# Optimization experiments

Hardware: AMD Instinct MI355X
Metric: run time of the kernel (lower is better)

The kernel has to match this reference:

```python
import jax, jax.numpy as jnp
import numpy as np

B, H, W, DIM, HEADS, WS, SHIFT, MLP_RATIO = 32, 56, 56, 256, 8, 7, 3, 4
N = WS * WS                      # tokens per window = 49
NW = (H // WS) * (W // WS)       # windows per image = 64
HEAD_DIM = DIM // HEADS
HIDDEN = DIM * MLP_RATIO


def _rel_index():
    # standard Swin relative position index, shape (N, N), values in [0, (2*WS-1)^2)
    coords = np.stack(np.meshgrid(np.arange(WS), np.arange(WS), indexing='ij')).reshape(2, -1)
    rel = (coords[:, :, None] - coords[:, None, :]).transpose(1, 2, 0)
    rel[:, :, 0] += WS - 1
    rel[:, :, 1] += WS - 1
    rel[:, :, 0] *= 2 * WS - 1
    return rel.sum(-1).astype(np.int32)


def _attn_mask():
    # shifted-window attention mask, shape (NW, N, N), values in {0, -100}
    img = np.zeros((H, W))
    slices = (slice(0, -WS), slice(-WS, -SHIFT), slice(-SHIFT, None))
    cnt = 0
    for hs in slices:
        for ws_ in slices:
            img[hs, ws_] = cnt
            cnt += 1
    mw = img.reshape(H // WS, WS, W // WS, WS).transpose(0, 2, 1, 3).reshape(-1, N)
    diff = mw[:, None, :] - mw[:, :, None]
    return np.where(diff != 0, -100.0, 0.0).astype(np.float32)


def setup_inputs() -> dict:
    key = jax.random.key(0)
    ks = jax.random.split(key, 16)
    s = 0.02
    return {
        'x': jax.random.normal(ks[0], (B, H * W, DIM), jnp.float32),
        'norm1_w': jnp.ones((DIM,), jnp.float32),
        'norm1_b': jnp.zeros((DIM,), jnp.float32),
        'qkv_w': jax.random.normal(ks[1], (3 * DIM, DIM), jnp.float32) * s,
        'qkv_b': jnp.zeros((3 * DIM,), jnp.float32),
        'rpb_table': jax.random.normal(ks[2], ((2 * WS - 1) ** 2, HEADS), jnp.float32) * s,
        'proj_w': jax.random.normal(ks[3], (DIM, DIM), jnp.float32) * s,
        'proj_b': jnp.zeros((DIM,), jnp.float32),
        'norm2_w': jnp.ones((DIM,), jnp.float32),
        'norm2_b': jnp.zeros((DIM,), jnp.float32),
        'fc1_w': jax.random.normal(ks[4], (HIDDEN, DIM), jnp.float32) * s,
        'fc1_b': jnp.zeros((HIDDEN,), jnp.float32),
        'fc2_w': jax.random.normal(ks[5], (DIM, HIDDEN), jnp.float32) * s,
        'fc2_b': jnp.zeros((DIM,), jnp.float32),
        'rel_idx': jnp.asarray(_rel_index()),
        'attn_mask': jnp.asarray(_attn_mask()),
    }


def _ln(t, w, b):
    mu = t.mean(-1, keepdims=True)
    var = ((t - mu) ** 2).mean(-1, keepdims=True)
    return (t - mu) * jax.lax.rsqrt(var + 1e-5) * w + b


def reference(x, norm1_w, norm1_b, qkv_w, qkv_b, rpb_table, proj_w, proj_b,
              norm2_w, norm2_b, fc1_w, fc1_b, fc2_w, fc2_b, rel_idx, attn_mask):
    Bz = x.shape[0]
    shortcut = x
    h = _ln(x, norm1_w, norm1_b).reshape(Bz, H, W, DIM)
    h = jnp.roll(h, (-SHIFT, -SHIFT), axis=(1, 2))                      # cyclic shift
    # window partition -> (Bz*NW, N, C)
    h = h.reshape(Bz, H // WS, WS, W // WS, WS, DIM).transpose(0, 1, 3, 2, 4, 5).reshape(-1, N, DIM)
    qkv = (h @ qkv_w.T + qkv_b).reshape(-1, N, 3, HEADS, HEAD_DIM).transpose(2, 0, 3, 1, 4)
    q, k, v = qkv[0], qkv[1], qkv[2]                                    # (Bz*NW, heads, N, d)
    scale = HEAD_DIM ** -0.5
    attn = jnp.einsum('whnd,whmd->whnm', q * scale, k)
    bias = rpb_table[rel_idx].transpose(2, 0, 1)                        # (heads, N, N)
    attn = attn + bias[None]
    attn = attn.reshape(Bz, NW, HEADS, N, N) + attn_mask[None, :, None]  # shift mask
    attn = jax.nn.softmax(attn.reshape(-1, HEADS, N, N), axis=-1)
    out = jnp.einsum('whnm,whmd->whnd', attn, v).transpose(0, 2, 1, 3).reshape(-1, N, DIM)
    out = out @ proj_w.T + proj_b
    # window reverse + un-shift
    out = out.reshape(Bz, H // WS, W // WS, WS, WS, DIM).transpose(0, 1, 3, 2, 4, 5).reshape(Bz, H, W, DIM)
    out = jnp.roll(out, (SHIFT, SHIFT), axis=(1, 2)).reshape(Bz, H * W, DIM)
    x = shortcut + out
    # residual MLP (pre-LN), exact GELU as in nn.GELU default
    h2 = _ln(x, norm2_w, norm2_b)
    h2 = jax.nn.gelu(h2 @ fc1_w.T + fc1_b, approximate=False)
    return x + (h2 @ fc2_w.T + fc2_b)
```

## Files before the change

kernel.cpp:

```cpp
#include <hip/hip_runtime.h>

typedef unsigned short ushort_t;
typedef __attribute__((ext_vector_type(8))) __bf16 bf16x8;
typedef __attribute__((ext_vector_type(4))) float floatx4;

#define TOKS 100352

__device__ __forceinline__ ushort_t f2bf(float f) {
    union { float f; unsigned u; } a; a.f = f;
    unsigned r = a.u + 0x7fffu + ((a.u >> 16) & 1u);
    return (ushort_t)(r >> 16);
}

__device__ __forceinline__ void async16(const void* g, void* l) {
    __builtin_amdgcn_global_load_lds(
        (const __attribute__((address_space(1))) unsigned int*)g,
        (__attribute__((address_space(3))) unsigned int*)l,
        16, 0, 0);
}

__device__ __forceinline__ int win_to_orig(int t) {
    int b = t / 3136, rr = t - b * 3136;
    int w_ = rr / 49, pos = rr - w_ * 49;
    int wi = w_ >> 3, wj = w_ & 7;
    int ti = pos / 7, tj = pos - ti * 7;
    int h = wi * 7 + ti + 3; if (h >= 56) h -= 56;
    int w = wj * 7 + tj + 3; if (w >= 56) w -= 56;
    return b * 3136 + h * 56 + w;
}

__global__ void convert_kernel(const float* __restrict__ qkv_w, const float* __restrict__ proj_w,
                               const float* __restrict__ fc1_w, const float* __restrict__ fc2_w,
                               const float* __restrict__ rpb, const int* __restrict__ rel_idx,
                               const float* __restrict__ amask,
                               ushort_t* __restrict__ wq, ushort_t* __restrict__ wp,
                               ushort_t* __restrict__ w1, ushort_t* __restrict__ w2,
                               float* __restrict__ bm) {
    int i = blockIdx.x * 256 + threadIdx.x;
    if (i < 196608) wq[i] = f2bf(qkv_w[i]);
    if (i < 65536)  wp[i] = f2bf(proj_w[i]);
    if (i < 262144) { w1[i] = f2bf(fc1_w[i]); w2[i] = f2bf(fc2_w[i]); }
    if (i < 1229312) {
        int wh = i / 2401, ij = i - wh * 2401;
        int head = wh & 7, wimg = wh >> 3;
        bm[i] = rpb[rel_idx[ij] * 8 + head] + amask[wimg * 2401 + ij];
    }
}

template <int GATHER>
__global__ __launch_bounds__(256) void ln_kernel(const float* __restrict__ xin,
                                                 const float* __restrict__ gw,
                                                 const float* __restrict__ gb,
                                                 ushort_t* __restrict__ outb) {
    const int wid = threadIdx.x >> 6, lane = threadIdx.x & 63;
    const int t_out = blockIdx.x * 4 + wid;
    const int t_in = GATHER ? win_to_orig(t_out) : t_out;
    const float4* src = (const float4*)(xin + (long)t_in * 256);
    float4 v = src[lane];
    float s  = v.x + v.y + v.z + v.w;
    float s2 = v.x*v.x + v.y*v.y + v.z*v.z + v.w*v.w;
    #pragma unroll
    for (int d = 32; d >= 1; d >>= 1) { s += __shfl_xor(s, d, 64); s2 += __shfl_xor(s2, d, 64); }
    float mu  = s * 0.00390625f;
    float var = s2 * 0.00390625f - mu * mu;
    float ry  = rsqrtf(var + 1e-5f);
    float4 w4 = ((const float4*)gw)[lane], b4 = ((const float4*)gb)[lane];
    unsigned long long p =
          (unsigned long long)f2bf((v.x - mu) * ry * w4.x + b4.x)
        | ((unsigned long long)f2bf((v.y - mu) * ry * w4.y + b4.y) << 16)
        | ((unsigned long long)f2bf((v.z - mu) * ry * w4.z + b4.z) << 32)
        | ((unsigned long long)f2bf((v.w - mu) * ry * w4.w + b4.w) << 48);
    ((unsigned long long*)(outb + (long)t_out * 256))[lane] = p;
}

template <int MODE, int N_LD, int KD>
__global__ __launch_bounds__(256, 2) void gemm_kernel(const ushort_t* __restrict__ A,
                                                      const ushort_t* __restrict__ Bw,
                                                      const float* __restrict__ bias,
                                                      void* __restrict__ outp) {
    __shared__ __align__(16) ushort_t As[128 * 32];
    __shared__ __align__(16) ushort_t Bs[128 * 32];
    const int tid = threadIdx.x;
    const int lane = tid & 63;
    const int wid = tid >> 6;
    const int wm = wid & 1, wn = wid >> 1;
    const int l15 = lane & 15, quad = lane >> 4;
    const long tileM = (long)blockIdx.y * 128;
    const long tileN = (long)blockIdx.x * 128;

    floatx4 acc[4][4];
    #pragma unroll
    for (int i = 0; i < 4; i++)
        #pragma unroll
        for (int j = 0; j < 4; j++) acc[i][j] = {0.f, 0.f, 0.f, 0.f};

    const int o1 = tid * 16;
    const int r1 = o1 >> 6, c1 = (o1 & 63) >> 1;
    const ushort_t* Ar1 = A + (tileM + r1) * KD + c1;
    const ushort_t* Ar2 = A + (tileM + r1 + 64) * KD + c1;
    const ushort_t* Br1 = Bw + (tileN + r1) * KD + c1;
    const ushort_t* Br2 = Bw + (tileN + r1 + 64) * KD + c1;
    ushort_t* Ad1 = &As[o1 >> 1];
    ushort_t* Ad2 = &As[(o1 >> 1) + 2048];
    ushort_t* Bd1 = &Bs[o1 >> 1];
    ushort_t* Bd2 = &Bs[(o1 >> 1) + 2048];

    for (int k0 = 0; k0 < KD; k0 += 32) {
        async16(Ar1 + k0, Ad1);
        async16(Ar2 + k0, Ad2);
        async16(Br1 + k0, Bd1);
        async16(Br2 + k0, Bd2);
        __syncthreads();
        bf16x8 af[4], bfr[4];
        #pragma unroll
        for (int mi = 0; mi < 4; mi++)
            af[mi] = *(const bf16x8*)&As[(wm * 64 + mi * 16 + l15) * 32 + quad * 8];
        #pragma unroll
        for (int nj = 0; nj < 4; nj++)
            bfr[nj] = *(const bf16x8*)&Bs[(wn * 64 + nj * 16 + l15) * 32 + quad * 8];
        #pragma unroll
        for (int mi = 0; mi < 4; mi++)
            #pragma unroll
            for (int nj = 0; nj < 4; nj++)
                acc[mi][nj] = __builtin_amdgcn_mfma_f32_16x16x32_bf16(af[mi], bfr[nj], acc[mi][nj], 0, 0, 0);
        __syncthreads();
    }

    #pragma unroll
    for (int mi = 0; mi < 4; mi++)
      #pragma unroll
      for (int nj = 0; nj < 4; nj++)
        #pragma unroll
        for (int r = 0; r < 4; r++) {
            long row = tileM + wm * 64 + mi * 16 + quad * 4 + r;
            long col = tileN + wn * 64 + nj * 16 + l15;
            float v = acc[mi][nj][r] + bias[col];
            if (MODE == 0) {
                ((ushort_t*)outp)[row * N_LD + col] = f2bf(v);
            } else if (MODE == 2) {
                float g = 0.5f * v * (1.f + erff(v * 0.70710678118654752f));
                ((ushort_t*)outp)[row * N_LD + col] = f2bf(g);
            } else {
                ((float*)outp)[row * N_LD + col] += v;
            }
        }
}

__global__ __launch_bounds__(256, 2) void proj_ln_kernel(
        const ushort_t* __restrict__ A, const ushort_t* __restrict__ Bw,
        const float* __restrict__ pb, const float* __restrict__ x_res,
        const float* __restrict__ n2w, const float* __restrict__ n2b,
        float* __restrict__ xout, ushort_t* __restrict__ h2out) {
    __shared__ __align__(16) ushort_t As[64 * 32];
    __shared__ __align__(16) ushort_t Bs[256 * 32];
    __shared__ float red_s[4][64];
    __shared__ float red_q[4][64];
    const int tid = threadIdx.x, lane = tid & 63, wid = tid >> 6;
    const int l15 = lane & 15, quad = lane >> 4;
    const long tileM = (long)blockIdx.x * 64;

    floatx4 acc[4][4];
    #pragma unroll
    for (int i = 0; i < 4; i++)
        #pragma unroll
        for (int j = 0; j < 4; j++) acc[i][j] = {0.f, 0.f, 0.f, 0.f};

    const int oA = tid * 16;
    const int rA = oA >> 6, cA = (oA & 63) >> 1;
    const ushort_t* Ap = A + (tileM + rA) * 256 + cA;
    ushort_t* Ad = &As[oA >> 1];

    for (int k0 = 0; k0 < 256; k0 += 32) {
        async16(Ap + k0, Ad);
        #pragma unroll
        for (int ch = 0; ch < 4; ch++) {
            int o = ch * 4096 + oA;
            async16(Bw + (o >> 6) * 256 + ((o & 63) >> 1) + k0, &Bs[o >> 1]);
        }
        __syncthreads();
        bf16x8 af[4], bfr[4];
        #pragma unroll
        for (int mi = 0; mi < 4; mi++)
            af[mi] = *(const bf16x8*)&As[(mi * 16 + l15) * 32 + quad * 8];
        #pragma unroll
        for (int nj = 0; nj < 4; nj++)
            bfr[nj] = *(const bf16x8*)&Bs[(wid * 64 + nj * 16 + l15) * 32 + quad * 8];
        #pragma unroll
        for (int mi = 0; mi < 4; mi++)
            #pragma unroll
            for (int nj = 0; nj < 4; nj++)
                acc[mi][nj] = __builtin_amdgcn_mfma_f32_16x16x32_bf16(af[mi], bfr[nj], acc[mi][nj], 0, 0, 0);
        __syncthreads();
    }

    int orig[4][4];
    #pragma unroll
    for (int mi = 0; mi < 4; mi++)
      #pragma unroll
      for (int r = 0; r < 4; r++) {
        int iloc = mi * 16 + quad * 4 + r;
        orig[mi][r] = win_to_orig((int)tileM + iloc);
        float s = 0.f, q = 0.f;
        #pragma unroll
        for (int nj = 0; nj < 4; nj++) {
            int col = wid * 64 + nj * 16 + l15;
            long gi = (long)orig[mi][r] * 256 + col;
            float v = acc[mi][nj][r] + pb[col] + x_res[gi];
            xout[gi] = v;
            acc[mi][nj][r] = v;
            s += v; q += v * v;
        }
        #pragma unroll
        for (int d = 1; d < 16; d <<= 1) { s += __shfl_xor(s, d, 64); q += __shfl_xor(q, d, 64); }
        if (l15 == 0) { red_s[wid][iloc] = s; red_q[wid][iloc] = q; }
      }
    __syncthreads();
    #pragma unroll
    for (int mi = 0; mi < 4; mi++)
      #pragma unroll
      for (int r = 0; r < 4; r++) {
        int iloc = mi * 16 + quad * 4 + r;
        float s = red_s[0][iloc] + red_s[1][iloc] + red_s[2][iloc] + red_s[3][iloc];
        float q = red_q[0][iloc] + red_q[1][iloc] + red_q[2][iloc] + red_q[3][iloc];
        float mu = s * 0.00390625f;
        float var = q * 0.00390625f - mu * mu;
        float rstd = rsqrtf(var + 1e-5f);
        #pragma unroll
        for (int nj = 0; nj < 4; nj++) {
            int col = wid * 64 + nj * 16 + l15;
            float v = acc[mi][nj][r];
            h2out[(long)orig[mi][r] * 256 + col] = f2bf((v - mu) * rstd * n2w[col] + n2b[col]);
        }
      }
}

__global__ __launch_bounds__(64) void attn_kernel(const ushort_t* __restrict__ qkv,
                                                  const float* __restrict__ bm,
                                                  ushort_t* __restrict__ attnout) {
    __shared__ __align__(16) ushort_t lds[96 * 72];
    ushort_t* Pl = lds;
    ushort_t* Vt = lds + 64 * 72;
    const int lane = threadIdx.x;
    const int whid = blockIdx.x;
    const int win = whid >> 3, head = whid & 7;
    const int l15 = lane & 15, quad = lane >> 4;
    const long base = (long)win * 49 * 768;
    const float* bmw = bm + (long)((win & 63) * 8 + head) * 2401;

    bf16x8 qf[4], kf[4];
    #pragma unroll
    for (int t4 = 0; t4 < 4; t4++) {
        int tok = t4 * 16 + l15; if (tok > 48) tok = 48;
        const ushort_t* p = qkv + base + (long)tok * 768 + head * 32 + quad * 8;
        qf[t4] = *(const bf16x8*)p;
        kf[t4] = *(const bf16x8*)(p + 256);
    }

    floatx4 S[4][4];
    #pragma unroll
    for (int mi = 0; mi < 4; mi++)
        #pragma unroll
        for (int nj = 0; nj < 4; nj++) {
            floatx4 z = {0.f, 0.f, 0.f, 0.f};
            S[mi][nj] = __builtin_amdgcn_mfma_f32_16x16x32_bf16(qf[mi], kf[nj], z, 0, 0, 0);
        }

    {
        int j = lane;
        int jc = j < 49 ? j : 48;
        const uint4* vsrc = (const uint4*)(qkv + base + (long)jc * 768 + 512 + head * 32);
        uint4 vz; vz.x = vz.y = vz.z = vz.w = 0u;
        #pragma unroll
        for (int q4 = 0; q4 < 4; q4++) {
            uint4 vv = (j < 49) ? vsrc[q4] : vz;
            int db = q4 * 8;
            Vt[(db+0)*72 + j] = (ushort_t)vv.x;  Vt[(db+1)*72 + j] = (ushort_t)(vv.x >> 16);
            Vt[(db+2)*72 + j] = (ushort_t)vv.y;  Vt[(db+3)*72 + j] = (ushort_t)(vv.y >> 16);
            Vt[(db+4)*72 + j] = (ushort_t)vv.z;  Vt[(db+5)*72 + j] = (ushort_t)(vv.z >> 16);
            Vt[(db+6)*72 + j] = (ushort_t)vv.w;  Vt[(db+7)*72 + j] = (ushort_t)(vv.w >> 16);
        }
    }

    const float scale = 0.17677669529663687f;
    #pragma unroll
    for (int mi = 0; mi < 4; mi++)
      #pragma unroll
      for (int nj = 0; nj < 4; nj++)
        #pragma unroll
        for (int r = 0; r < 4; r++) {
            int i = mi * 16 + quad * 4 + r;
            int j = nj * 16 + l15;
            float s = -1e30f;
            if (i < 49 && j < 49) s = S[mi][nj][r] * scale + bmw[i * 49 + j];
            S[mi][nj][r] = s;
        }

    float rinv[4][4];
    #pragma unroll
    for (int mi = 0; mi < 4; mi++)
      #pragma unroll
      for (int r = 0; r < 4; r++) {
          float m = fmaxf(fmaxf(S[mi][0][r], S[mi][1][r]), fmaxf(S[mi][2][r], S[mi][3][r]));
          #pragma unroll
          for (int d = 1; d < 16; d <<= 1) m = fmaxf(m, __shfl_xor(m, d, 64));
          float e[4], sum = 0.f;
          #pragma unroll
          for (int nj = 0; nj < 4; nj++) { e[nj] = __expf(S[mi][nj][r] - m); sum += e[nj]; }
          #pragma unroll
          for (int d = 1; d < 16; d <<= 1) sum += __shfl_xor(sum, d, 64);
          rinv[mi][r] = 1.f / sum;
          int i = mi * 16 + quad * 4 + r;
          #pragma unroll
          for (int nj = 0; nj < 4; nj++) Pl[i * 72 + (nj * 16 + l15)] = f2bf(e[nj]);
      }

    __syncthreads();

    floatx4 O[4][2];
    #pragma unroll
    for (int mi = 0; mi < 4; mi++) { O[mi][0] = {0.f,0.f,0.f,0.f}; O[mi][1] = {0.f,0.f,0.f,0.f}; }
    #pragma unroll
    for (int kc = 0; kc < 2; kc++) {
        bf16x8 pf[4], vf[2];
        #pragma unroll
        for (int mi = 0; mi < 4; mi++)
            pf[mi] = *(const bf16x8*)&Pl[(mi * 16 + l15) * 72 + kc * 32 + quad * 8];
        #pragma unroll
        for (int n2 = 0; n2 < 2; n2++)
            vf[n2] = *(const bf16x8*)&Vt[(n2 * 16 + l15) * 72 + kc * 32 + quad * 8];
        #pragma unroll
        for (int mi = 0; mi < 4; mi++)
            #pragma unroll
            for (int n2 = 0; n2 < 2; n2++)
                O[mi][n2] = __builtin_amdgcn_mfma_f32_16x16x32_bf16(pf[mi], vf[n2], O[mi][n2], 0, 0, 0);
    }

    #pragma unroll
    for (int mi = 0; mi < 4; mi++)
      #pragma unroll
      for (int n2 = 0; n2 < 2; n2++)
        #pragma unroll
        for (int r = 0; r < 4; r++) {
            int i = mi * 16 + quad * 4 + r;
            if (i < 49) {
                long orow = ((long)win * 49 + i) * 256 + head * 32 + n2 * 16 + l15;
                attnout[orow] = f2bf(O[mi][n2][r] * rinv[mi][r]);
            }
        }
}

extern "C" void kernel_launch(void* const* d_in, const int* in_sizes, int n_in,
                              void* d_out, int out_size, void* d_ws, size_t ws_size,
                              hipStream_t stream) {
    const float* x      = (const float*)d_in[0];
    const float* n1w    = (const float*)d_in[1];
    const float* n1b    = (const float*)d_in[2];
    const float* qkv_w  = (const float*)d_in[3];
    const float* qkv_b  = (const float*)d_in[4];
    const float* rpb    = (const float*)d_in[5];
    const float* proj_w = (const float*)d_in[6];
    const float* proj_b = (const float*)d_in[7];
    const float* n2w    = (const float*)d_in[8];
    const float* n2b    = (const float*)d_in[9];
    const float* fc1_w  = (const float*)d_in[10];
    const float* fc1_b  = (const float*)d_in[11];
    const float* fc2_w  = (const float*)d_in[12];
    const float* fc2_b  = (const float*)d_in[13];
    const int*   rel_idx= (const int*)d_in[14];
    const float* amask  = (const float*)d_in[15];

    char* ws = (char*)d_ws;
    ushort_t* wq   = (ushort_t*)(ws + 0);
    ushort_t* wp   = (ushort_t*)(ws + 393216);
    ushort_t* w1   = (ushort_t*)(ws + 524288);
    ushort_t* w2   = (ushort_t*)(ws + 1048576);
    ushort_t* hwin = (ushort_t*)(ws + 1572864);
    ushort_t* qkvb = (ushort_t*)(ws + 52953088);
    ushort_t* h2   = qkvb;
    ushort_t* h3   = (ushort_t*)(ws + 104333312);
    float* bm = (float*)d_out;

    convert_kernel<<<4803, 256, 0, stream>>>(qkv_w, proj_w, fc1_w, fc2_w, rpb, rel_idx,
                                             amask, wq, wp, w1, w2, bm);
    ln_kernel<1><<<TOKS / 4, 256, 0, stream>>>(x, n1w, n1b, hwin);
    gemm_kernel<0, 768, 256><<<dim3(6, 784), 256, 0, stream>>>(hwin, wq, qkv_b, qkvb);
    attn_kernel<<<16384, 64, 0, stream>>>(qkvb, bm, hwin);
    proj_ln_kernel<<<1568, 256, 0, stream>>>(hwin, wp, proj_b, x, n2w, n2b, (float*)d_out, h2);
    for (int c = 0; c < 2; c++) {
        gemm_kernel<2, 1024, 256><<<dim3(8, 392), 256, 0, stream>>>(
            h2 + (long)c * 50176 * 256, w1, fc1_b, h3);
        gemm_kernel<3, 256, 1024><<<dim3(2, 392), 256, 0, stream>>>(
            h3, w2, fc2_b, (float*)d_out + (long)c * 50176 * 256);
    }
    (void)in_sizes; (void)n_in; (void)out_size; (void)ws_size;
}
```

Baseline: 760.1 us.

## Keep residual in window order as bf16 and split bias/mask tables

The proj+LN kernel now writes the post-attention residual as bf16 in window order instead of scattering an fp32 copy into the output, and LN2's output also stays in window order. The fc2 GEMM then reads that bf16 residual and scatters the final result to the original token positions, so the read-modify-write of the fp32 output goes away. The combined bias+mask table (about 4.9 MB) is replaced by a small per-head bias table plus the raw mask, and the attention kernel runs two heads per 128-thread block. In exchange the residual is rounded to bf16, which costs accuracy, and the final stores become scattered by window.

```diff
diff --git a/kernel.cpp b/kernel.cpp
--- a/kernel.cpp
+++ b/kernel.cpp
@@ -32,29 +32,26 @@
 __global__ void convert_kernel(const float* __restrict__ qkv_w, const float* __restrict__ proj_w,
                                const float* __restrict__ fc1_w, const float* __restrict__ fc2_w,
                                const float* __restrict__ rpb, const int* __restrict__ rel_idx,
-                               const float* __restrict__ amask,
                                ushort_t* __restrict__ wq, ushort_t* __restrict__ wp,
                                ushort_t* __restrict__ w1, ushort_t* __restrict__ w2,
-                               float* __restrict__ bm) {
+                               float* __restrict__ bias_h) {
     int i = blockIdx.x * 256 + threadIdx.x;
     if (i < 196608) wq[i] = f2bf(qkv_w[i]);
     if (i < 65536)  wp[i] = f2bf(proj_w[i]);
     if (i < 262144) { w1[i] = f2bf(fc1_w[i]); w2[i] = f2bf(fc2_w[i]); }
-    if (i < 1229312) {
-        int wh = i / 2401, ij = i - wh * 2401;
-        int head = wh & 7, wimg = wh >> 3;
-        bm[i] = rpb[rel_idx[ij] * 8 + head] + amask[wimg * 2401 + ij];
-    }
-}
-
-template <int GATHER>
+    if (i < 19208) {
+        int h = i / 2401, ij = i - h * 2401;
+        bias_h[i] = rpb[rel_idx[ij] * 8 + h];
+    }
+}
+
 __global__ __launch_bounds__(256) void ln_kernel(const float* __restrict__ xin,
                                                  const float* __restrict__ gw,
                                                  const float* __restrict__ gb,
                                                  ushort_t* __restrict__ outb) {
     const int wid = threadIdx.x >> 6, lane = threadIdx.x & 63;
     const int t_out = blockIdx.x * 4 + wid;
-    const int t_in = GATHER ? win_to_orig(t_out) : t_out;
+    const int t_in = win_to_orig(t_out);
     const float4* src = (const float4*)(xin + (long)t_in * 256);
     float4 v = src[lane];
     float s  = v.x + v.y + v.z + v.w;
@@ -77,7 +74,9 @@
 __global__ __launch_bounds__(256, 2) void gemm_kernel(const ushort_t* __restrict__ A,
                                                       const ushort_t* __restrict__ Bw,
                                                       const float* __restrict__ bias,
-                                                      void* __restrict__ outp) {
+                                                      void* __restrict__ outp,
+                                                      const ushort_t* __restrict__ x1w,
+                                                      int rowOff) {
     __shared__ __align__(16) ushort_t As[128 * 32];
     __shared__ __align__(16) ushort_t Bs[128 * 32];
     const int tid = threadIdx.x;
@@ -141,7 +140,11 @@
                 float g = 0.5f * v * (1.f + erff(v * 0.70710678118654752f));
                 ((ushort_t*)outp)[row * N_LD + col] = f2bf(g);
             } else {
-                ((float*)outp)[row * N_LD + col] += v;
+                union { ushort_t u[2]; unsigned v32; float f; } cvt;
+                cvt.u[0] = 0; cvt.u[1] = x1w[row * 256 + col];
+                float res = cvt.f;
+                int orig = win_to_orig((int)row + rowOff);
+                ((float*)outp)[(long)orig * 256 + col] = v + res;
             }
         }
 }
@@ -150,7 +153,7 @@
         const ushort_t* __restrict__ A, const ushort_t* __restrict__ Bw,
         const float* __restrict__ pb, const float* __restrict__ x_res,
         const float* __restrict__ n2w, const float* __restrict__ n2b,
-        float* __restrict__ xout, ushort_t* __restrict__ h2out) {
+        ushort_t* __restrict__ x1w, ushort_t* __restrict__ h2out) {
     __shared__ __align__(16) ushort_t As[64 * 32];
     __shared__ __align__(16) ushort_t Bs[256 * 32];
     __shared__ float red_s[4][64];
@@ -193,20 +196,18 @@
         __syncthreads();
     }
 
-    int orig[4][4];
     #pragma unroll
     for (int mi = 0; mi < 4; mi++)
       #pragma unroll
       for (int r = 0; r < 4; r++) {
         int iloc = mi * 16 + quad * 4 + r;
-        orig[mi][r] = win_to_orig((int)tileM + iloc);
+        int orig = win_to_orig((int)tileM + iloc);
         float s = 0.f, q = 0.f;
         #pragma unroll
         for (int nj = 0; nj < 4; nj++) {
             int col = wid * 64 + nj * 16 + l15;
-            long gi = (long)orig[mi][r] * 256 + col;
-            float v = acc[mi][nj][r] + pb[col] + x_res[gi];
-            xout[gi] = v;
+            float v = acc[mi][nj][r] + pb[col] + x_res[(long)orig * 256 + col];
+            x1w[(tileM + iloc) * 256 + col] = f2bf(v);
             acc[mi][nj][r] = v;
             s += v; q += v * v;
         }
@@ -229,23 +230,25 @@
         for (int nj = 0; nj < 4; nj++) {
             int col = wid * 64 + nj * 16 + l15;
             float v = acc[mi][nj][r];
-            h2out[(long)orig[mi][r] * 256 + col] = f2bf((v - mu) * rstd * n2w[col] + n2b[col]);
+            h2out[(tileM + iloc) * 256 + col] = f2bf((v - mu) * rstd * n2w[col] + n2b[col]);
         }
       }
 }
 
-__global__ __launch_bounds__(64) void attn_kernel(const ushort_t* __restrict__ qkv,
-                                                  const float* __restrict__ bm,
-                                                  ushort_t* __restrict__ attnout) {
-    __shared__ __align__(16) ushort_t lds[96 * 72];
-    ushort_t* Pl = lds;
-    ushort_t* Vt = lds + 64 * 72;
-    const int lane = threadIdx.x;
-    const int whid = blockIdx.x;
+__global__ __launch_bounds__(128) void attn_kernel(const ushort_t* __restrict__ qkv,
+                                                   const float* __restrict__ bias_h,
+                                                   const float* __restrict__ mask,
+                                                   ushort_t* __restrict__ attnout) {
+    __shared__ __align__(16) ushort_t lds[2 * 6912];
+    const int tid = threadIdx.x, lane = tid & 63, wid = tid >> 6;
+    ushort_t* Pl = &lds[wid * 6912];
+    ushort_t* Vt = Pl + 64 * 72;
+    const int whid = blockIdx.x * 2 + wid;
     const int win = whid >> 3, head = whid & 7;
     const int l15 = lane & 15, quad = lane >> 4;
     const long base = (long)win * 49 * 768;
-    const float* bmw = bm + (long)((win & 63) * 8 + head) * 2401;
+    const float* bh = bias_h + head * 2401;
+    const float* mk = mask + (win & 63) * 2401;
 
     bf16x8 qf[4], kf[4];
     #pragma unroll
@@ -291,7 +294,10 @@
             int i = mi * 16 + quad * 4 + r;
             int j = nj * 16 + l15;
             float s = -1e30f;
-            if (i < 49 && j < 49) s = S[mi][nj][r] * scale + bmw[i * 49 + j];
+            if (i < 49 && j < 49) {
+                int ij = i * 49 + j;
+                s = S[mi][nj][r] * scale + bh[ij] + mk[ij];
+            }
             S[mi][nj][r] = s;
         }
 
@@ -374,23 +380,24 @@
     ushort_t* wp   = (ushort_t*)(ws + 393216);
     ushort_t* w1   = (ushort_t*)(ws + 524288);
     ushort_t* w2   = (ushort_t*)(ws + 1048576);
-    ushort_t* hwin = (ushort_t*)(ws + 1572864);
-    ushort_t* qkvb = (ushort_t*)(ws + 52953088);
-    ushort_t* h2   = qkvb;
-    ushort_t* h3   = (ushort_t*)(ws + 104333312);
-    float* bm = (float*)d_out;
-
-    convert_kernel<<<4803, 256, 0, stream>>>(qkv_w, proj_w, fc1_w, fc2_w, rpb, rel_idx,
-                                             amask, wq, wp, w1, w2, bm);
-    ln_kernel<1><<<TOKS / 4, 256, 0, stream>>>(x, n1w, n1b, hwin);
-    gemm_kernel<0, 768, 256><<<dim3(6, 784), 256, 0, stream>>>(hwin, wq, qkv_b, qkvb);
-    attn_kernel<<<16384, 64, 0, stream>>>(qkvb, bm, hwin);
-    proj_ln_kernel<<<1568, 256, 0, stream>>>(hwin, wp, proj_b, x, n2w, n2b, (float*)d_out, h2);
+    float*    bh   = (float*)   (ws + 1572864);
+    ushort_t* hwin = (ushort_t*)(ws + 1649728);
+    ushort_t* qkvb = (ushort_t*)(ws + 53029952);
+    ushort_t* h2   = (ushort_t*)(ws + 104410176);
+    ushort_t* x1w  = (ushort_t*)(ws + 155790400);
+    ushort_t* h3   = hwin;
+
+    convert_kernel<<<1024, 256, 0, stream>>>(qkv_w, proj_w, fc1_w, fc2_w, rpb, rel_idx,
+                                             wq, wp, w1, w2, bh);
+    ln_kernel<<<TOKS / 4, 256, 0, stream>>>(x, n1w, n1b, hwin);
+    gemm_kernel<0, 768, 256><<<dim3(6, 784), 256, 0, stream>>>(hwin, wq, qkv_b, qkvb, nullptr, 0);
+    attn_kernel<<<8192, 128, 0, stream>>>(qkvb, bh, amask, hwin);
+    proj_ln_kernel<<<1568, 256, 0, stream>>>(hwin, wp, proj_b, x, n2w, n2b, x1w, h2);
     for (int c = 0; c < 2; c++) {
         gemm_kernel<2, 1024, 256><<<dim3(8, 392), 256, 0, stream>>>(
-            h2 + (long)c * 50176 * 256, w1, fc1_b, h3);
-        gemm_kernel<3, 256, 1024><<<dim3(2, 392), 256, 0, stream>>>(
-            h3, w2, fc2_b, (float*)d_out + (long)c * 50176 * 256);
+            h2 + (long)c * 50176 * 256, w1, fc1_b, h3, nullptr, 0);
+        gemm_kernel<4, 256, 1024><<<dim3(2, 392), 256, 0, stream>>>(
+            h3, w2, fc2_b, (float*)d_out, x1w + (long)c * 50176 * 256, c * 50176);
     }
     (void)in_sizes; (void)n_in; (void)out_size; (void)ws_size;
 }
```

After: 750.7 us. Within noise of the previous version (-1.2%).
